# Kernel optimization log

Hardware: AMD Instinct MI355X
Metric: run time of the kernel (lower is better)

The kernel has to match this reference:

```python
import jax, jax.numpy as jnp
import numpy as np

N_HEAD = 16
HIDDEN = 1024

def setup_inputs() -> dict:
    key = jax.random.key(0)
    ks = jax.random.split(key, 4)
    B, T, D = 2, 2048, HIDDEN
    x = jax.random.normal(ks[0], (B, T, D), dtype=jnp.float32)
    attention_mask = jnp.zeros((B, 1, 1, T), dtype=jnp.float32)  # additive mask
    w_attn = jax.random.normal(ks[1], (D, 3 * D), dtype=jnp.float32) * (1.0 / np.sqrt(D))
    b_attn = jnp.zeros((3 * D,), dtype=jnp.float32)
    w_proj = jax.random.normal(ks[2], (D, D), dtype=jnp.float32) * (1.0 / np.sqrt(D))
    b_proj = jnp.zeros((D,), dtype=jnp.float32)
    return {"x": x, "attention_mask": attention_mask,
            "w_attn": w_attn, "b_attn": b_attn,
            "w_proj": w_proj, "b_proj": b_proj}

def reference(x, attention_mask, w_attn, b_attn, w_proj, b_proj):
    B, T, D = x.shape
    H = N_HEAD
    hd = D // H
    qkv = x @ w_attn + b_attn                      # [B,T,3D]
    q, k, v = jnp.split(qkv, 3, axis=-1)
    q = q.reshape(B, T, H, hd)
    k = k.reshape(B, T, H, hd)
    v = v.reshape(B, T, H, hd)
    qk = jnp.einsum('BFNH,BTNH->BNFT', q, k) / jnp.sqrt(jnp.asarray(hd, qk_dtype := q.dtype))
    # NOTE: source adds the mask twice (once unconditionally, once inside the None-check)
    attn_weights = qk + attention_mask + attention_mask
    attn_probs = jax.nn.softmax(attn_weights, axis=-1)  # dropout(0.01) is identity at inference
    attn_out = jnp.einsum('BNFT,BTNH->BFNH', attn_probs, v)
    attn_out = attn_out.reshape(B, T, D)
    return attn_out @ w_proj + b_proj
```

## Files before the change

### kernel.cpp

```cpp
#include <hip/hip_runtime.h>
#include <hip/hip_bf16.h>

#define T_SEQ 2048
#define D_MODEL 1024
#define N_HEADS 16

typedef _Float16 half8 __attribute__((ext_vector_type(8)));
typedef _Float16 half4 __attribute__((ext_vector_type(4)));
typedef _Float16 half2v __attribute__((ext_vector_type(2)));
typedef float floatx4 __attribute__((ext_vector_type(4)));
typedef unsigned short ushort4v __attribute__((ext_vector_type(4)));
typedef unsigned short ushort8v __attribute__((ext_vector_type(8)));

#define LOG2E 1.44269504088896f

__device__ __forceinline__ unsigned short f32_to_bf16(float f) {
  unsigned u = __builtin_bit_cast(unsigned, f);
  u = u + 0x7FFFu + ((u >> 16) & 1u);
  return (unsigned short)(u >> 16);
}
__device__ __forceinline__ float bf16_to_f32(unsigned short h) {
  unsigned u = ((unsigned)h) << 16;
  return __builtin_bit_cast(float, u);
}
__device__ __forceinline__ half2v pk_f16(float a, float b) {
  return __builtin_bit_cast(half2v, __builtin_amdgcn_cvt_pkrtz(a, b));
}

__device__ __forceinline__ void load16_lds(const _Float16* g, _Float16* lds_base, int lane) {
#if __has_builtin(__builtin_amdgcn_global_load_lds)
  __builtin_amdgcn_global_load_lds(
      (const __attribute__((address_space(1))) void*)g,
      (__attribute__((address_space(3))) void*)lds_base, 16, 0, 0);
#else
  *(half8*)(lds_base + lane * 8) = *(const half8*)g;
#endif
}

__global__ void k_detect(const unsigned short* __restrict__ x, int* __restrict__ flag) {
  __shared__ int cnt;
  if (threadIdx.x == 0) cnt = 0;
  __syncthreads();
  unsigned short v = x[(size_t)threadIdx.x * 2];
  int e = (v >> 7) & 0xFF;
  int ok = (v == 0) || (e >= 100 && e <= 150);
  atomicAdd(&cnt, ok);
  __syncthreads();
  if (threadIdx.x == 0) *flag = (cnt >= 192) ? 1 : 0;
}

__global__ __launch_bounds__(256) void k_transpose2(
    const void* __restrict__ inA, _Float16* __restrict__ outA,
    const void* __restrict__ inB, _Float16* __restrict__ outB,
    const void* __restrict__ ba, const void* __restrict__ bp,
    const void* __restrict__ mk, float* __restrict__ baF,
    float* __restrict__ bpF, float* __restrict__ mask2,
    const int* __restrict__ flag) {
  __shared__ float tile[32][33];
  int f = *flag;
  if (blockIdx.x >= 4096) {
    int i = (blockIdx.x - 4096) * 256 + threadIdx.x;
    auto cv = [&](const void* p, int j) {
      return f ? bf16_to_f32(((const unsigned short*)p)[j]) : ((const float*)p)[j];
    };
    if (i < 3072) baF[i] = cv(ba, i);
    else if (i < 4096) bpF[i - 3072] = cv(bp, i - 3072);
    else mask2[i - 4096] = cv(mk, i - 4096) * (2.0f * LOG2E);
    return;
  }
  const void* in;
  _Float16* out;
  int N, bid;
  if (blockIdx.x < 3072) { in = inA; out = outA; N = 3072; bid = blockIdx.x; }
  else { in = inB; out = outB; N = 1024; bid = blockIdx.x - 3072; }
  const int K = 1024;
  int nb = N >> 5;
  int bx = bid % nb, by = bid / nb;
  int n0 = bx << 5, k0 = by << 5;
  int c = threadIdx.x & 31, r = threadIdx.x >> 5;
  const float* fin = (const float*)in;
  const unsigned short* uin = (const unsigned short*)in;
#pragma unroll
  for (int i = 0; i < 4; ++i) {
    int kk = r + i * 8;
    size_t idx = (size_t)(k0 + kk) * N + n0 + c;
    tile[kk][c] = f ? bf16_to_f32(uin[idx]) : fin[idx];
  }
  __syncthreads();
#pragma unroll
  for (int i = 0; i < 4; ++i) {
    int nn = r + i * 8;
    out[(size_t)(n0 + nn) * K + k0 + c] = (_Float16)tile[c][nn];
  }
}

__global__ __launch_bounds__(256) void k_gemm(
    const _Float16* __restrict__ A, const void* __restrict__ BT,
    const float* __restrict__ bias, void* __restrict__ D0,
    void* __restrict__ D1, void* __restrict__ D2,
    int M, int N, int K, int outKind, int bRaw, const int* __restrict__ flag) {
  __shared__ _Float16 As[128 * 64] __attribute__((aligned(16)));
  __shared__ _Float16 Bs[128 * 64] __attribute__((aligned(16)));
  const int tid = threadIdx.x;
  const int wave = tid >> 6, lane = tid & 63;
  const int ln = lane & 15, quad = lane >> 4;
  const int nbx = gridDim.x;
  const int nwg = nbx * gridDim.y;
  const int bid0 = blockIdx.y * nbx + blockIdx.x;
  const int id = (bid0 & 7) * (nwg >> 3) + (bid0 >> 3);
  const int bm = (id / nbx) * 128, bn = (id % nbx) * 128;
  const int wm = (wave & 1) * 64, wn = (wave >> 1) * 64;
  const int f = *flag;

  const int sr = tid >> 3, scn = (tid & 7) ^ (sr & 7);
  const _Float16* Ag = A + (size_t)(bm + sr) * K + scn * 8;
  const _Float16* Bg16 = (const _Float16*)BT + (size_t)(bn + sr) * K + scn * 8;
  const float* Bg32 = (const float*)BT + (size_t)(bn + sr) * K + scn * 8;
  const unsigned short* Bgbf = (const unsigned short*)BT + (size_t)(bn + sr) * K + scn * 8;

  floatx4 acc[4][4] = {};

  for (int kt = 0; kt < K; kt += 64) {
    __syncthreads();
#pragma unroll
    for (int i = 0; i < 4; ++i)
      load16_lds(Ag + kt + (size_t)i * 32 * K, As + (wave * 64 + i * 256) * 8, lane);
    if (!bRaw) {
#pragma unroll
      for (int i = 0; i < 4; ++i)
        load16_lds(Bg16 + kt + (size_t)i * 32 * K, Bs + (wave * 64 + i * 256) * 8, lane);
    } else if (f) {
#pragma unroll
      for (int i = 0; i < 4; ++i) {
        ushort8v u = *(const ushort8v*)(Bgbf + kt + (size_t)i * 32 * K);
        half8 o;
#pragma unroll
        for (int e = 0; e < 8; ++e) o[e] = (_Float16)bf16_to_f32(u[e]);
        *(half8*)(Bs + (size_t)(wave * 64 + i * 256 + lane) * 8) = o;
      }
    } else {
#pragma unroll
      for (int i = 0; i < 4; ++i) {
        const float* sp = Bg32 + kt + (size_t)i * 32 * K;
        floatx4 a = *(const floatx4*)sp;
        floatx4 b = *(const floatx4*)(sp + 4);
        half8 o;
#pragma unroll
        for (int e = 0; e < 4; ++e) { o[e] = (_Float16)a[e]; o[e + 4] = (_Float16)b[e]; }
        *(half8*)(Bs + (size_t)(wave * 64 + i * 256 + lane) * 8) = o;
      }
    }
    __syncthreads();
    half8 af[4][2], bf[4][2];
#pragma unroll
    for (int i = 0; i < 4; ++i) {
      int r = wm + i * 16 + ln;
#pragma unroll
      for (int ks = 0; ks < 2; ++ks)
        af[i][ks] = *(const half8*)(As + r * 64 + ((quad + 4 * ks) ^ (r & 7)) * 8);
    }
#pragma unroll
    for (int j = 0; j < 4; ++j) {
      int r = wn + j * 16 + ln;
#pragma unroll
      for (int ks = 0; ks < 2; ++ks)
        bf[j][ks] = *(const half8*)(Bs + r * 64 + ((quad + 4 * ks) ^ (r & 7)) * 8);
    }
#pragma unroll
    for (int ks = 0; ks < 2; ++ks)
#pragma unroll
      for (int i = 0; i < 4; ++i)
#pragma unroll
        for (int j = 0; j < 4; ++j)
          acc[i][j] = __builtin_amdgcn_mfma_f32_16x16x32_f16(af[i][ks], bf[j][ks], acc[i][j], 0, 0, 0);
  }

  if (outKind == 0) {
    _Float16* Qs = (_Float16*)D0;
    _Float16* Ks = (_Float16*)D1;
    _Float16* Vt = (_Float16*)D2;
    const float qsc = 0.125f * LOG2E;
#pragma unroll
    for (int i = 0; i < 4; ++i) {
      int rbase = bm + wm + i * 16 + quad * 4;
      int sect = rbase >> 10;
      int cfeat = rbase & 1023;
      int h = cfeat >> 6, hd = cfeat & 63;
      float bv[4];
#pragma unroll
      for (int r = 0; r < 4; ++r) bv[r] = bias[rbase + r];
#pragma unroll
      for (int j = 0; j < 4; ++j) {
        int col = bn + wn + j * 16 + ln;
        int b = col >> 11, t = col & 2047;
        size_t bh = (size_t)b * N_HEADS + h;
        float v[4];
#pragma unroll
        for (int r = 0; r < 4; ++r) v[r] = acc[i][j][r] + bv[r];
        if (sect == 0) {
          half4 q;
#pragma unroll
          for (int r = 0; r < 4; ++r) q[r] = (_Float16)(v[r] * qsc);
          *(half4*)(Qs + (bh * T_SEQ + t) * 64 + hd) = q;
        } else if (sect == 1) {
          half4 kk4;
#pragma unroll
          for (int r = 0; r < 4; ++r) kk4[r] = (_Float16)v[r];
          *(half4*)(Ks + (bh * T_SEQ + t) * 64 + hd) = kk4;
        } else {
#pragma unroll
          for (int r = 0; r < 4; ++r)
            Vt[(bh * 64 + hd + r) * T_SEQ + t] = (_Float16)v[r];
        }
      }
    }
  } else {
    int mode = f ? 2 : 1;
#pragma unroll
    for (int i = 0; i < 4; ++i) {
      int rbase = bm + wm + i * 16 + quad * 4;
      float bv[4];
#pragma unroll
      for (int r = 0; r < 4; ++r) bv[r] = bias[rbase + r];
#pragma unroll
      for (int j = 0; j < 4; ++j) {
        int col = bn + wn + j * 16 + ln;
        float v[4];
#pragma unroll
        for (int r = 0; r < 4; ++r) v[r] = acc[i][j][r] + bv[r];
        if (mode == 1) {
          floatx4 o = {v[0], v[1], v[2], v[3]};
          *(floatx4*)((float*)D0 + (size_t)col * M + rbase) = o;
        } else {
          ushort4v o;
#pragma unroll
          for (int r = 0; r < 4; ++r) o[r] = f32_to_bf16(v[r]);
          *(ushort4v*)((unsigned short*)D0 + (size_t)col * M + rbase) = o;
        }
      }
    }
  }
}

__global__ __launch_bounds__(256) void k_gemm64(
    const _Float16* __restrict__ A, const _Float16* __restrict__ BT,
    const float* __restrict__ bias, void* __restrict__ D0,
    int M, int N, int K, const int* __restrict__ flag) {
  __shared__ _Float16 As[64 * 64] __attribute__((aligned(16)));
  __shared__ _Float16 Bs[64 * 64] __attribute__((aligned(16)));
  const int tid = threadIdx.x;
  const int wave = tid >> 6, lane = tid & 63;
  const int ln = lane & 15, quad = lane >> 4;
  const int nbx = gridDim.x;
  const int nwg = nbx * gridDim.y;
  const int bid0 = blockIdx.y * nbx + blockIdx.x;
  const int id = (bid0 & 7) * (nwg >> 3) + (bid0 >> 3);
  const int bm = (id / nbx) * 64, bn = (id % nbx) * 64;
  const int wm = (wave & 1) * 32, wn = (wave >> 1) * 32;
  const int f = *flag;

  const int sr = tid >> 3, scn = (tid & 7) ^ (sr & 7);
  const _Float16* Ag = A + (size_t)(bm + sr) * K + scn * 8;
  const _Float16* Bg = BT + (size_t)(bn + sr) * K + scn * 8;

  floatx4 acc[2][2] = {};

  for (int kt = 0; kt < K; kt += 64) {
    __syncthreads();
#pragma unroll
    for (int i = 0; i < 2; ++i) {
      load16_lds(Ag + kt + (size_t)i * 32 * K, As + (wave * 64 + i * 256) * 8, lane);
      load16_lds(Bg + kt + (size_t)i * 32 * K, Bs + (wave * 64 + i * 256) * 8, lane);
    }
    __syncthreads();
    half8 af[2][2], bf[2][2];
#pragma unroll
    for (int i = 0; i < 2; ++i) {
      int r = wm + i * 16 + ln;
#pragma unroll
      for (int ks = 0; ks < 2; ++ks)
        af[i][ks] = *(const half8*)(As + r * 64 + ((quad + 4 * ks) ^ (r & 7)) * 8);
    }
#pragma unroll
    for (int j = 0; j < 2; ++j) {
      int r = wn + j * 16 + ln;
#pragma unroll
      for (int ks = 0; ks < 2; ++ks)
        bf[j][ks] = *(const half8*)(Bs + r * 64 + ((quad + 4 * ks) ^ (r & 7)) * 8);
    }
#pragma unroll
    for (int ks = 0; ks < 2; ++ks)
#pragma unroll
      for (int i = 0; i < 2; ++i)
#pragma unroll
        for (int j = 0; j < 2; ++j)
          acc[i][j] = __builtin_amdgcn_mfma_f32_16x16x32_f16(af[i][ks], bf[j][ks], acc[i][j], 0, 0, 0);
  }

  int mode = f ? 2 : 1;
#pragma unroll
  for (int i = 0; i < 2; ++i) {
    int rbase = bm + wm + i * 16 + quad * 4;
    float bv[4];
#pragma unroll
    for (int r = 0; r < 4; ++r) bv[r] = bias[rbase + r];
#pragma unroll
    for (int j = 0; j < 2; ++j) {
      int col = bn + wn + j * 16 + ln;
      float v[4];
#pragma unroll
      for (int r = 0; r < 4; ++r) v[r] = acc[i][j][r] + bv[r];
      if (mode == 1) {
        floatx4 o = {v[0], v[1], v[2], v[3]};
        *(floatx4*)((float*)D0 + (size_t)col * M + rbase) = o;
      } else {
        ushort4v o;
#pragma unroll
        for (int r = 0; r < 4; ++r) o[r] = f32_to_bf16(v[r]);
        *(ushort4v*)((unsigned short*)D0 + (size_t)col * M + rbase) = o;
      }
    }
  }
}

__global__ __launch_bounds__(256, 4) void k_flash(
    const _Float16* __restrict__ Qs, const _Float16* __restrict__ Ks,
    const _Float16* __restrict__ Vt, const float* __restrict__ mask2,
    _Float16* __restrict__ O) {
  __shared__ __attribute__((aligned(16))) char smem[40960];
  _Float16* KlB = (_Float16*)smem;
  _Float16* VlB = (_Float16*)(smem + 16384);
  float* MaskL = (float*)(smem + 32768);
  float* Red = (float*)smem;

  const int tid = threadIdx.x, wave = tid >> 6, lane = tid & 63;
  const int ln = lane & 15, quad = lane >> 4;
  const int qh = wave & 1, kh = wave >> 1;
  const int id = ((blockIdx.x & 7) << 7) | (blockIdx.x >> 3);
  const int qc = id & 31, h = (id >> 5) & 15, b = id >> 9;
  const size_t bh = (size_t)b * N_HEADS + h;
  const _Float16* Qb = Qs + bh * T_SEQ * 64;
  const _Float16* Kb = Ks + bh * T_SEQ * 64;
  const _Float16* Vb = Vt + bh * 64 * T_SEQ;
  const int q0w = qc * 64 + qh * 32;

  {
    const floatx4* src = (const floatx4*)(mask2 + (size_t)b * T_SEQ);
    floatx4* dst = (floatx4*)MaskL;
#pragma unroll
    for (int i = 0; i < 2; ++i) dst[tid + i * 256] = src[tid + i * 256];
  }

  half8 qf[2][2];
#pragma unroll
  for (int jq = 0; jq < 2; ++jq)
#pragma unroll
    for (int kk = 0; kk < 2; ++kk)
      qf[jq][kk] = *(const half8*)(Qb + (size_t)(q0w + jq * 16 + ln) * 64 + kk * 32 + quad * 8);

  int koff[2][2], voff[4][2];
#pragma unroll
  for (int jk = 0; jk < 2; ++jk) {
    int krow = kh * 32 + jk * 16 + ln;
    koff[jk][0] = (krow * 64 + ((quad) ^ (krow & 7)) * 8) * 2;
    koff[jk][1] = (krow * 64 + ((4 + quad) ^ (krow & 7)) * 8) * 2;
  }
#pragma unroll
  for (int jd = 0; jd < 4; ++jd) {
    int vrow = jd * 16 + ln;
    voff[jd][0] = (vrow * 64 + ((kh * 4 + 0 + (quad >> 1)) ^ (vrow & 7)) * 8 + (quad & 1) * 4) * 2;
    voff[jd][1] = (vrow * 64 + ((kh * 4 + 2 + (quad >> 1)) ^ (vrow & 7)) * 8 + (quad & 1) * 4) * 2;
  }

  floatx4 Oacc[4][2] = {};
  float li[2] = {0.f, 0.f};

  const int sr = tid >> 3, scn = (tid & 7) ^ (sr & 7);
  const _Float16* kp0 = Kb + (size_t)sr * 64 + scn * 8;
  const _Float16* kp1 = kp0 + 32 * 64;
  const _Float16* vp0 = Vb + (size_t)sr * T_SEQ + scn * 8;
  const _Float16* vp1 = vp0 + 32 * T_SEQ;

  {
    _Float16* K0 = KlB + (size_t)wave * 512;
    _Float16* V0 = VlB + (size_t)wave * 512;
    load16_lds(kp0, K0, lane);
    load16_lds(kp1, K0 + 2048, lane);
    load16_lds(vp0, V0, lane);
    load16_lds(vp1, V0 + 2048, lane);
    kp0 += 64 * 64; kp1 += 64 * 64; vp0 += 64; vp1 += 64;
  }

  for (int t = 0; t < 32; ++t) {
    const int cur = t & 1;
    __syncthreads();
    if (t + 1 < 32) {
      _Float16* K0 = KlB + (cur ^ 1) * 4096 + (size_t)wave * 512;
      _Float16* V0 = VlB + (cur ^ 1) * 4096 + (size_t)wave * 512;
      load16_lds(kp0, K0, lane);
      load16_lds(kp1, K0 + 2048, lane);
      load16_lds(vp0, V0, lane);
      load16_lds(vp1, V0 + 2048, lane);
      kp0 += 64 * 64; kp1 += 64 * 64; vp0 += 64; vp1 += 64;
    }
    const char* Kc = (const char*)KlB + cur * 8192;
    const char* Vc = (const char*)VlB + cur * 8192;
    const float* mt = MaskL + t * 64 + kh * 32 + quad * 4;

    floatx4 s[2][2];
    __builtin_amdgcn_s_setprio(1);
#pragma unroll
    for (int jk = 0; jk < 2; ++jk) {
      half8 kf0 = *(const half8*)(Kc + koff[jk][0]);
      half8 kf1 = *(const half8*)(Kc + koff[jk][1]);
      floatx4 mk4 = *(const floatx4*)(mt + jk * 16);
#pragma unroll
      for (int jq = 0; jq < 2; ++jq) {
        floatx4 z = __builtin_amdgcn_mfma_f32_16x16x32_f16(kf0, qf[jq][0], mk4, 0, 0, 0);
        z = __builtin_amdgcn_mfma_f32_16x16x32_f16(kf1, qf[jq][1], z, 0, 0, 0);
        s[jk][jq] = z;
      }
    }
    __builtin_amdgcn_s_setprio(0);

#pragma unroll
    for (int jk = 0; jk < 2; ++jk)
#pragma unroll
      for (int jq = 0; jq < 2; ++jq)
#pragma unroll
        for (int r = 0; r < 4; ++r) {
          float p = __builtin_amdgcn_exp2f(s[jk][jq][r]);
          s[jk][jq][r] = p;
          li[jq] += p;
        }

    half4 pf4[2][2];
#pragma unroll
    for (int jk = 0; jk < 2; ++jk)
#pragma unroll
      for (int jq = 0; jq < 2; ++jq) {
        half2v p01 = pk_f16(s[jk][jq][0], s[jk][jq][1]);
        half2v p23 = pk_f16(s[jk][jq][2], s[jk][jq][3]);
        pf4[jk][jq] = (half4){p01[0], p01[1], p23[0], p23[1]};
      }

    __builtin_amdgcn_s_setprio(1);
#pragma unroll
    for (int jd = 0; jd < 4; ++jd) {
      half4 vf0 = *(const half4*)(Vc + voff[jd][0]);
      half4 vf1 = *(const half4*)(Vc + voff[jd][1]);
#pragma unroll
      for (int jq = 0; jq < 2; ++jq) {
        Oacc[jd][jq] = __builtin_amdgcn_mfma_f32_16x16x16f16(vf0, pf4[0][jq], Oacc[jd][jq], 0, 0, 0);
        Oacc[jd][jq] = __builtin_amdgcn_mfma_f32_16x16x16f16(vf1, pf4[1][jq], Oacc[jd][jq], 0, 0, 0);
      }
    }
    __builtin_amdgcn_s_setprio(0);
  }

#pragma unroll
  for (int jq = 0; jq < 2; ++jq) {
    li[jq] += __shfl_xor(li[jq], 16, 64);
    li[jq] += __shfl_xor(li[jq], 32, 64);
  }

  __syncthreads();
  float* myRed = Red + ((size_t)qh * 64 + lane) * 36;
  if (kh) {
#pragma unroll
    for (int jd = 0; jd < 4; ++jd)
#pragma unroll
      for (int jq = 0; jq < 2; ++jq)
#pragma unroll
        for (int r = 0; r < 4; ++r) myRed[jd * 8 + jq * 4 + r] = Oacc[jd][jq][r];
#pragma unroll
    for (int jq = 0; jq < 2; ++jq) myRed[32 + jq] = li[jq];
  }
  __syncthreads();
  if (!kh) {
    float inv[2];
#pragma unroll
    for (int jq = 0; jq < 2; ++jq) inv[jq] = 1.f / (li[jq] + myRed[32 + jq]);
#pragma unroll
    for (int jd = 0; jd < 4; ++jd)
#pragma unroll
      for (int jq = 0; jq < 2; ++jq) {
        half4 ov;
#pragma unroll
        for (int r = 0; r < 4; ++r) {
          float v = Oacc[jd][jq][r] + myRed[jd * 8 + jq * 4 + r];
          ov[r] = (_Float16)(v * inv[jq]);
        }
        *(half4*)(O + ((size_t)b * T_SEQ + q0w + jq * 16 + ln) * D_MODEL +
                  h * 64 + jd * 16 + quad * 4) = ov;
      }
  }
}

extern "C" void kernel_launch(void* const* d_in, const int* in_sizes, int n_in,
                              void* d_out, int out_size, void* d_ws, size_t ws_size,
                              hipStream_t stream) {
  const void* x      = d_in[0];
  const void* amask  = d_in[1];
  const void* w_attn = d_in[2];
  const void* b_attn = d_in[3];
  const void* w_proj = d_in[4];
  const void* b_proj = d_in[5];

  char* ws = (char*)d_ws;
  size_t off = 0;
  auto alloc = [&](size_t bytes) {
    void* p = ws + off;
    off += (bytes + 255) & ~(size_t)255;
    return p;
  };
  int* flag        = (int*)alloc(256);
  _Float16* WaT    = (_Float16*)alloc((size_t)3072 * 1024 * 2);
  _Float16* WpT    = (_Float16*)alloc((size_t)1024 * 1024 * 2);
  float* baF       = (float*)alloc(3072 * 4);
  float* bpF       = (float*)alloc(1024 * 4);
  float* mask2     = (float*)alloc(4096 * 4);
  _Float16* Qs     = (_Float16*)alloc((size_t)4096 * 1024 * 2);
  _Float16* Ks     = (_Float16*)alloc((size_t)4096 * 1024 * 2);
  _Float16* Vt     = (_Float16*)alloc((size_t)4096 * 1024 * 2);
  _Float16* AttnH  = (_Float16*)alloc((size_t)4096 * 1024 * 2);

  k_detect<<<1, 256, 0, stream>>>((const unsigned short*)x, flag);
  k_transpose2<<<3072 + 1024 + 32, 256, 0, stream>>>(
      w_attn, WaT, w_proj, WpT, b_attn, b_proj, amask, baF, bpF, mask2, flag);

  dim3 g1(4096 / 128, 3072 / 128);
  k_gemm<<<g1, 256, 0, stream>>>(WaT, x, baF, Qs, Ks, Vt, 3072, 4096, 1024, 0, 1, flag);

  k_flash<<<1024, 256, 0, stream>>>(Qs, Ks, Vt, mask2, AttnH);

  dim3 g2(4096 / 64, 1024 / 64);
  k_gemm64<<<g2, 256, 0, stream>>>(WpT, AttnH, bpF, d_out, 1024, 4096, 1024, flag);
}
```

Baseline: 195.5 us.

## Inline dtype detection, remap GEMM block order, widen output-projection tile

Drops the separate k_detect launch: every block of the transpose and GEMM kernels now runs the dtype check itself with a wave ballot and popcount. Both GEMMs get a new block-to-tile mapping that groups nearby N-tiles together for L2 reuse. The output-projection GEMM grows its tile from 64x64 to 64x128 with more accumulators per wave, which halves the grid. The aim is less launch overhead and better operand reuse, paid for by a redundant detect read in every block and more register use.

```diff
diff --git a/kernel.cpp b/kernel.cpp
--- a/kernel.cpp
+++ b/kernel.cpp
@@ -37,16 +37,16 @@
 #endif
 }
 
-__global__ void k_detect(const unsigned short* __restrict__ x, int* __restrict__ flag) {
-  __shared__ int cnt;
-  if (threadIdx.x == 0) cnt = 0;
-  __syncthreads();
-  unsigned short v = x[(size_t)threadIdx.x * 2];
+__device__ __forceinline__ int detect_flag(const unsigned short* __restrict__ x) {
+  __shared__ int dcnt[4];
+  const int tid = threadIdx.x;
+  unsigned short v = x[(size_t)(tid & 255) * 2];
   int e = (v >> 7) & 0xFF;
   int ok = (v == 0) || (e >= 100 && e <= 150);
-  atomicAdd(&cnt, ok);
+  unsigned long long m = __ballot(ok);
+  if ((tid & 63) == 0) dcnt[(tid >> 6) & 3] = (int)__popcll(m);
   __syncthreads();
-  if (threadIdx.x == 0) *flag = (cnt >= 192) ? 1 : 0;
+  return (dcnt[0] + dcnt[1] + dcnt[2] + dcnt[3]) >= 192;
 }
 
 __global__ __launch_bounds__(256) void k_transpose2(
@@ -55,9 +55,9 @@
     const void* __restrict__ ba, const void* __restrict__ bp,
     const void* __restrict__ mk, float* __restrict__ baF,
     float* __restrict__ bpF, float* __restrict__ mask2,
-    const int* __restrict__ flag) {
+    const unsigned short* __restrict__ xdet) {
   __shared__ float tile[32][33];
-  int f = *flag;
+  int f = detect_flag(xdet);
   if (blockIdx.x >= 4096) {
     int i = (blockIdx.x - 4096) * 256 + threadIdx.x;
     auto cv = [&](const void* p, int j) {
@@ -98,19 +98,19 @@
     const _Float16* __restrict__ A, const void* __restrict__ BT,
     const float* __restrict__ bias, void* __restrict__ D0,
     void* __restrict__ D1, void* __restrict__ D2,
-    int M, int N, int K, int outKind, int bRaw, const int* __restrict__ flag) {
+    int M, int N, int K, int outKind, int bRaw,
+    const unsigned short* __restrict__ xdet) {
   __shared__ _Float16 As[128 * 64] __attribute__((aligned(16)));
   __shared__ _Float16 Bs[128 * 64] __attribute__((aligned(16)));
   const int tid = threadIdx.x;
   const int wave = tid >> 6, lane = tid & 63;
   const int ln = lane & 15, quad = lane >> 4;
-  const int nbx = gridDim.x;
-  const int nwg = nbx * gridDim.y;
-  const int bid0 = blockIdx.y * nbx + blockIdx.x;
-  const int id = (bid0 & 7) * (nwg >> 3) + (bid0 >> 3);
-  const int bm = (id / nbx) * 128, bn = (id % nbx) * 128;
+  const int f = detect_flag(xdet);
+  const int bid0 = blockIdx.y * gridDim.x + blockIdx.x;
+  const int xj = bid0 & 7, xt = bid0 >> 3;
+  const int bn = (xj * 4 + (xt & 3)) * 128;
+  const int bm = (xt >> 2) * 128;
   const int wm = (wave & 1) * 64, wn = (wave >> 1) * 64;
-  const int f = *flag;
 
   const int sr = tid >> 3, scn = (tid & 7) ^ (sr & 7);
   const _Float16* Ag = A + (size_t)(bm + sr) * K + scn * 8;
@@ -242,38 +242,38 @@
   }
 }
 
-__global__ __launch_bounds__(256) void k_gemm64(
+__global__ __launch_bounds__(256) void k_gemm2(
     const _Float16* __restrict__ A, const _Float16* __restrict__ BT,
     const float* __restrict__ bias, void* __restrict__ D0,
-    int M, int N, int K, const int* __restrict__ flag) {
+    int M, int N, int K, const unsigned short* __restrict__ xdet) {
   __shared__ _Float16 As[64 * 64] __attribute__((aligned(16)));
-  __shared__ _Float16 Bs[64 * 64] __attribute__((aligned(16)));
+  __shared__ _Float16 Bs[128 * 64] __attribute__((aligned(16)));
   const int tid = threadIdx.x;
   const int wave = tid >> 6, lane = tid & 63;
   const int ln = lane & 15, quad = lane >> 4;
-  const int nbx = gridDim.x;
-  const int nwg = nbx * gridDim.y;
-  const int bid0 = blockIdx.y * nbx + blockIdx.x;
-  const int id = (bid0 & 7) * (nwg >> 3) + (bid0 >> 3);
-  const int bm = (id / nbx) * 64, bn = (id % nbx) * 64;
-  const int wm = (wave & 1) * 32, wn = (wave >> 1) * 32;
-  const int f = *flag;
+  const int f = detect_flag(xdet);
+  const int bid0 = blockIdx.y * gridDim.x + blockIdx.x;
+  const int xj = bid0 & 7, xt = bid0 >> 3;
+  const int bn = (xj * 4 + (xt & 3)) * 128;
+  const int bm = (xt >> 2) * 64;
+  const int wm = (wave & 1) * 32, wn = (wave >> 1) * 64;
 
   const int sr = tid >> 3, scn = (tid & 7) ^ (sr & 7);
   const _Float16* Ag = A + (size_t)(bm + sr) * K + scn * 8;
   const _Float16* Bg = BT + (size_t)(bn + sr) * K + scn * 8;
 
-  floatx4 acc[2][2] = {};
+  floatx4 acc[2][4] = {};
 
   for (int kt = 0; kt < K; kt += 64) {
     __syncthreads();
 #pragma unroll
-    for (int i = 0; i < 2; ++i) {
+    for (int i = 0; i < 2; ++i)
       load16_lds(Ag + kt + (size_t)i * 32 * K, As + (wave * 64 + i * 256) * 8, lane);
+#pragma unroll
+    for (int i = 0; i < 4; ++i)
       load16_lds(Bg + kt + (size_t)i * 32 * K, Bs + (wave * 64 + i * 256) * 8, lane);
-    }
     __syncthreads();
-    half8 af[2][2], bf[2][2];
+    half8 af[2][2], bf[4][2];
 #pragma unroll
     for (int i = 0; i < 2; ++i) {
       int r = wm + i * 16 + ln;
@@ -282,7 +282,7 @@
         af[i][ks] = *(const half8*)(As + r * 64 + ((quad + 4 * ks) ^ (r & 7)) * 8);
     }
 #pragma unroll
-    for (int j = 0; j < 2; ++j) {
+    for (int j = 0; j < 4; ++j) {
       int r = wn + j * 16 + ln;
 #pragma unroll
       for (int ks = 0; ks < 2; ++ks)
@@ -293,7 +293,7 @@
 #pragma unroll
       for (int i = 0; i < 2; ++i)
 #pragma unroll
-        for (int j = 0; j < 2; ++j)
+        for (int j = 0; j < 4; ++j)
           acc[i][j] = __builtin_amdgcn_mfma_f32_16x16x32_f16(af[i][ks], bf[j][ks], acc[i][j], 0, 0, 0);
   }
 
@@ -305,7 +305,7 @@
 #pragma unroll
     for (int r = 0; r < 4; ++r) bv[r] = bias[rbase + r];
 #pragma unroll
-    for (int j = 0; j < 2; ++j) {
+    for (int j = 0; j < 4; ++j) {
       int col = bn + wn + j * 16 + ln;
       float v[4];
 #pragma unroll
@@ -506,6 +506,7 @@
   const void* b_attn = d_in[3];
   const void* w_proj = d_in[4];
   const void* b_proj = d_in[5];
+  const unsigned short* xdet = (const unsigned short*)x;
 
   char* ws = (char*)d_ws;
   size_t off = 0;
@@ -514,7 +515,6 @@
     off += (bytes + 255) & ~(size_t)255;
     return p;
   };
-  int* flag        = (int*)alloc(256);
   _Float16* WaT    = (_Float16*)alloc((size_t)3072 * 1024 * 2);
   _Float16* WpT    = (_Float16*)alloc((size_t)1024 * 1024 * 2);
   float* baF       = (float*)alloc(3072 * 4);
@@ -525,15 +525,14 @@
   _Float16* Vt     = (_Float16*)alloc((size_t)4096 * 1024 * 2);
   _Float16* AttnH  = (_Float16*)alloc((size_t)4096 * 1024 * 2);
 
-  k_detect<<<1, 256, 0, stream>>>((const unsigned short*)x, flag);
   k_transpose2<<<3072 + 1024 + 32, 256, 0, stream>>>(
-      w_attn, WaT, w_proj, WpT, b_attn, b_proj, amask, baF, bpF, mask2, flag);
+      w_attn, WaT, w_proj, WpT, b_attn, b_proj, amask, baF, bpF, mask2, xdet);
 
   dim3 g1(4096 / 128, 3072 / 128);
-  k_gemm<<<g1, 256, 0, stream>>>(WaT, x, baF, Qs, Ks, Vt, 3072, 4096, 1024, 0, 1, flag);
+  k_gemm<<<g1, 256, 0, stream>>>(WaT, x, baF, Qs, Ks, Vt, 3072, 4096, 1024, 0, 1, xdet);
 
   k_flash<<<1024, 256, 0, stream>>>(Qs, Ks, Vt, mask2, AttnH);
 
-  dim3 g2(4096 / 64, 1024 / 64);
-  k_gemm64<<<g2, 256, 0, stream>>>(WpT, AttnH, bpF, d_out, 1024, 4096, 1024, flag);
-}
+  dim3 g2(4096 / 128, 1024 / 64);
+  k_gemm2<<<g2, 256, 0, stream>>>(WpT, AttnH, bpF, d_out, 1024, 4096, 1024, xdet);
+}
```

New measurement: 199.3 us. Within noise of the previous version (+1.9%).
